# Kernel optimization log

Measured on AMD Instinct MI355X. Metric: run time of the kernel, lower is better.

Reference implementation:

```python
import jax, jax.numpy as jnp
import numpy as np

NUM_HEADS = 16


def setup_inputs() -> dict:
    key = jax.random.key(0)
    ks = jax.random.split(key, 8)
    B, S, E = 2, 2048, 1024
    std = 0.02
    return {
        "q": jax.random.normal(ks[0], (B, S, E), dtype=jnp.float32),
        "k": jax.random.normal(ks[1], (B, S, E), dtype=jnp.float32),
        "v": jax.random.normal(ks[2], (B, S, E), dtype=jnp.float32),
        "Wq": jax.random.normal(ks[3], (E, E), dtype=jnp.float32) * std,
        "Wk": jax.random.normal(ks[4], (E, E), dtype=jnp.float32) * std,
        "Wv": jax.random.normal(ks[5], (E, E), dtype=jnp.float32) * std,
        "Wo": jax.random.normal(ks[6], (E, E), dtype=jnp.float32) * std,
        "bo": jnp.zeros((E,), dtype=jnp.float32),
    }


def reference(q, k, v, Wq, Wk, Wv, Wo, bo):
    B, S, E = q.shape
    H = NUM_HEADS
    D = E // H
    # projections (nn.Linear: x @ W.T)
    Q = (q @ Wq.T).reshape(B, S, H, D).transpose(0, 2, 1, 3)  # [B,H,S,D]
    K = (k @ Wk.T).reshape(B, S, H, D).transpose(0, 2, 1, 3)
    V = (v @ Wv.T).reshape(B, S, H, D).transpose(0, 2, 1, 3)
    scores = jnp.einsum("bhsd,bhtd->bhst", Q, K)  # [B,H,S,S]
    # causal mask applied before scaling (as in source; -inf/sqrt(d) == -inf)
    causal = jnp.tril(jnp.ones((S, S), dtype=bool))
    scores = jnp.where(causal, scores, -jnp.inf)
    scores = scores / np.sqrt(D).astype(np.float32)
    attn = jax.nn.softmax(scores, axis=-1)
    out = jnp.einsum("bhst,bhtd->bhsd", attn, V)  # [B,H,S,D]
    out = out.transpose(0, 2, 1, 3).reshape(B, S, E)
    return out @ Wo.T + bo
```

## Files before the change

kernel.cpp:

```cpp
#include <hip/hip_runtime.h>

typedef unsigned short u16;
typedef __bf16 bf16x8 __attribute__((ext_vector_type(8)));
typedef float f32x4 __attribute__((ext_vector_type(4)));
typedef unsigned u32x4 __attribute__((ext_vector_type(4)));

#define B_ 2
#define S_ 2048
#define E_ 1024
#define H_ 16
#define D_ 64
#define M_ (B_ * S_)

__device__ inline u16 f2bf(float f) {
  union { float f; unsigned int u; } c; c.f = f;
  unsigned int u = c.u;
  return (u16)((u + 0x7FFFu + ((u >> 16) & 1u)) >> 16);
}

__device__ inline f32x4 mfma16(bf16x8 a, bf16x8 b, f32x4 c) {
  return __builtin_amdgcn_mfma_f32_16x16x32_bf16(a, b, c, 0, 0, 0);
}

__device__ inline void gload16(const void* g, void* lds) {
  __builtin_amdgcn_global_load_lds(
      (const __attribute__((address_space(1))) unsigned int*)g,
      (__attribute__((address_space(3))) unsigned int*)lds, 16, 0, 0);
}

struct CvtArgs {
  const float* src[7];
  u16* dst[7];
  int n[7];
};

__global__ __launch_bounds__(256) void cvt_kernel(CvtArgs a) {
  const int arr = blockIdx.y;
  const int n = a.n[arr];
  const float* __restrict__ s = a.src[arr];
  u16* __restrict__ d = a.dst[arr];
  const int stride = gridDim.x * blockDim.x;
  for (int i = blockIdx.x * blockDim.x + threadIdx.x; i * 4 < n; i += stride) {
    const float4 f = *(const float4*)(s + 4 * i);
    ushort4 o;
    o.x = f2bf(f.x); o.y = f2bf(f.y); o.z = f2bf(f.z); o.w = f2bf(f.w);
    *(ushort4*)(d + 4 * i) = o;
  }
}

__global__ __launch_bounds__(256, 4) void qkv_gemm(
    const u16* __restrict__ qb, const u16* __restrict__ kb,
    const u16* __restrict__ vbp, const u16* __restrict__ Wqb,
    const u16* __restrict__ Wkb, const u16* __restrict__ Wvb,
    u16* __restrict__ Qh, u16* __restrict__ Kh, u16* __restrict__ Vt) {
  constexpr int BM = 128, BN = 128, BK = 32;
  __shared__ alignas(16) u16 As[BM * BK];
  __shared__ alignas(16) u16 Bs[BN * BK];
  const int z = blockIdx.z;
  const u16* A  = (z == 0) ? qb  : (z == 1) ? kb  : vbp;
  const u16* Bt = (z == 0) ? Wqb : (z == 1) ? Wkb : Wvb;
  u16* outp     = (z == 0) ? Qh  : (z == 1) ? Kh  : Vt;

  const int tid = threadIdx.x;
  const int wave = tid >> 6, lane = tid & 63;
  const int m0 = blockIdx.y * BM, n0 = blockIdx.x * BN;
  const int wm = (wave >> 1) * 64, wn = (wave & 1) * 64;
  const int lrow = lane >> 2, lcol = (lane & 3) * 8;

  f32x4 acc[4][4] = {};

  for (int k0 = 0; k0 < E_; k0 += BK) {
#pragma unroll
    for (int i = 0; i < 2; ++i) {
      const int chunk = wave * 2 + i;
      const int row = chunk * 16 + lrow;
      gload16(A + (size_t)(m0 + row) * E_ + k0 + lcol, As + chunk * 16 * BK);
      gload16(Bt + (size_t)(n0 + row) * E_ + k0 + lcol, Bs + chunk * 16 * BK);
    }
    __syncthreads();
    bf16x8 af[4], bfr[4];
#pragma unroll
    for (int mi = 0; mi < 4; ++mi)
      af[mi] = *(const bf16x8*)&As[(wm + mi * 16 + (lane & 15)) * BK + 8 * (lane >> 4)];
#pragma unroll
    for (int ni = 0; ni < 4; ++ni)
      bfr[ni] = *(const bf16x8*)&Bs[(wn + ni * 16 + (lane & 15)) * BK + 8 * (lane >> 4)];
#pragma unroll
    for (int mi = 0; mi < 4; ++mi)
#pragma unroll
      for (int ni = 0; ni < 4; ++ni)
        acc[mi][ni] = mfma16(af[mi], bfr[ni], acc[mi][ni]);
    __syncthreads();
  }

#pragma unroll
  for (int mi = 0; mi < 4; ++mi)
#pragma unroll
    for (int ni = 0; ni < 4; ++ni)
#pragma unroll
      for (int r = 0; r < 4; ++r) {
        const int m = m0 + wm + mi * 16 + ((lane >> 4) << 2) + r;
        const int n = n0 + wn + ni * 16 + (lane & 15);
        const float v = acc[mi][ni][r];
        const int b = m >> 11, s = m & (S_ - 1), h = n >> 6, d = n & 63;
        if (z != 2) {
          outp[((((size_t)b * H_ + h) * S_ + s) << 6) + d] = f2bf(v);
        } else {
          outp[(((size_t)b * H_ + h) * D_ + d) * S_ + s] = f2bf(v);
        }
      }
}

__global__ __launch_bounds__(256, 4) void oproj_gemm(
    const u16* __restrict__ A, const u16* __restrict__ Bt,
    const float* __restrict__ bias, float* __restrict__ outp) {
  constexpr int BM = 64, BN = 128, BK = 32;
  constexpr int ACH = BM / 16, NCH = ACH + BN / 16;
  __shared__ alignas(16) u16 As[BM * BK];
  __shared__ alignas(16) u16 Bs[BN * BK];
  const int tid = threadIdx.x;
  const int wave = tid >> 6, lane = tid & 63;
  const int m0 = blockIdx.y * BM, n0 = blockIdx.x * BN;
  const int wm = (wave >> 1) * 32, wn = (wave & 1) * 64;
  const int lrow = lane >> 2, lcol = (lane & 3) * 8;

  f32x4 acc[2][4] = {};

  for (int k0 = 0; k0 < E_; k0 += BK) {
#pragma unroll
    for (int c = wave; c < NCH; c += 4) {
      if (c < ACH)
        gload16(A + (size_t)(m0 + c * 16 + lrow) * E_ + k0 + lcol, As + c * 16 * BK);
      else
        gload16(Bt + (size_t)(n0 + (c - ACH) * 16 + lrow) * E_ + k0 + lcol,
                Bs + (c - ACH) * 16 * BK);
    }
    __syncthreads();
    bf16x8 af[2], bfr[4];
#pragma unroll
    for (int mi = 0; mi < 2; ++mi)
      af[mi] = *(const bf16x8*)&As[(wm + mi * 16 + (lane & 15)) * BK + 8 * (lane >> 4)];
#pragma unroll
    for (int ni = 0; ni < 4; ++ni)
      bfr[ni] = *(const bf16x8*)&Bs[(wn + ni * 16 + (lane & 15)) * BK + 8 * (lane >> 4)];
#pragma unroll
    for (int mi = 0; mi < 2; ++mi)
#pragma unroll
      for (int ni = 0; ni < 4; ++ni)
        acc[mi][ni] = mfma16(af[mi], bfr[ni], acc[mi][ni]);
    __syncthreads();
  }

#pragma unroll
  for (int mi = 0; mi < 2; ++mi)
#pragma unroll
    for (int ni = 0; ni < 4; ++ni)
#pragma unroll
      for (int r = 0; r < 4; ++r) {
        const int m = m0 + wm + mi * 16 + ((lane >> 4) << 2) + r;
        const int n = n0 + wn + ni * 16 + (lane & 15);
        outp[(size_t)m * E_ + n] = acc[mi][ni][r] + bias[n];
      }
}


__device__ __forceinline__ void stage_kv(
    const u16* __restrict__ Kh_head, const u16* __restrict__ Vt_head,
    int kv0, u16* kb, u16* vb, int wq, int lane) {
#pragma unroll
  for (int i = 0; i < 2; ++i) {
    const int c = 2 * wq + i;
    gload16(Kh_head + (size_t)(kv0 + lane) * D_ + c * 8, kb + c * 512);
    gload16(Vt_head + (size_t)lane * S_ + kv0 + c * 8, vb + c * 512);
  }
}

__global__ __launch_bounds__(256, 2) void flash_attn(
    const u16* __restrict__ Qh, const u16* __restrict__ Kh,
    const u16* __restrict__ Vt, u16* __restrict__ O) {
  __shared__ alignas(16) u16 Kb[3][4096];
  __shared__ alignas(16) u16 Vb[3][4096];

  const int j = blockIdx.x;
  const int qt = 31 - (j >> 5);
  const int bh = j & 31;

  const int tid = threadIdx.x;
  const int wq = tid >> 6, lane = tid & 63;

  const int q0 = qt * 64;
  const int b = bh >> 4, h = bh & 15;
  constexpr float SC = 0.125f * 1.4426950408889634f;
  const int fr = lane & 15, fc = lane >> 4;

  const u16* Qbase = Qh + ((size_t)bh * S_ + q0 + wq * 16 + fr) * D_ + 8 * fc;
  const bf16x8 qf0 = *(const bf16x8*)Qbase;
  const bf16x8 qf1 = *(const bf16x8*)(Qbase + 32);
  const u16* Kh_head = Kh + (size_t)bh * S_ * D_;
  const u16* Vt_head = Vt + (size_t)bh * D_ * S_;

  float lacc = 0.f;
  f32x4 oacc[4] = {};
  const int nt = qt + 1;

  u16 *kA = Kb[0], *kB = Kb[1], *kC = Kb[2];
  u16 *vA = Vb[0], *vB = Vb[1], *vC = Vb[2];

  stage_kv(Kh_head, Vt_head, 0, kA, vA, wq, lane);
  stage_kv(Kh_head, Vt_head, 64, kB, vB, wq, lane);

  for (int t = 0; t < nt; ++t) {
    if (t + 1 < nt) {
      asm volatile("s_waitcnt vmcnt(4)" ::: "memory");
    } else {
      asm volatile("s_waitcnt vmcnt(0)" ::: "memory");
    }
    __builtin_amdgcn_s_barrier();
    __builtin_amdgcn_sched_barrier(0);

    if (t + 2 < nt)
      stage_kv(Kh_head, Vt_head, (t + 2) * 64, kC, vC, wq, lane);

    const u16* kb = kA;
    const u16* vb = vA;

    f32x4 sacc[4] = {};
    __builtin_amdgcn_s_setprio(1);
#pragma unroll
    for (int ni = 0; ni < 4; ++ni) {
      const bf16x8 k0 = *(const bf16x8*)&kb[fc * 512 + (16 * ni + fr) * 8];
      const bf16x8 k1 = *(const bf16x8*)&kb[(fc + 4) * 512 + (16 * ni + fr) * 8];
      sacc[ni] = mfma16(k0, qf0, sacc[ni]);
      sacc[ni] = mfma16(k1, qf1, sacc[ni]);
    }
    __builtin_amdgcn_s_setprio(0);

    const bool diag = (t == qt);
    const int qloc = wq * 16 + fr;
#pragma unroll
    for (int ni = 0; ni < 4; ++ni)
#pragma unroll
      for (int r = 0; r < 4; ++r) {
        const int kvloc = 16 * ni + 4 * fc + r;
        float pv;
        if (diag && kvloc > qloc) {
          pv = 0.f;
        } else {
          pv = __builtin_amdgcn_exp2f(sacc[ni][r] * SC);
        }
        sacc[ni][r] = pv;
        lacc += pv;
      }

    unsigned w[4][2];
#pragma unroll
    for (int ni = 0; ni < 4; ++ni) {
      asm("v_cvt_pk_bf16_f32 %0, %1, %2"
          : "=v"(w[ni][0]) : "v"(sacc[ni][0]), "v"(sacc[ni][1]));
      asm("v_cvt_pk_bf16_f32 %0, %1, %2"
          : "=v"(w[ni][1]) : "v"(sacc[ni][2]), "v"(sacc[ni][3]));
    }

    unsigned paw0[4], paw1[4];
#pragma unroll
    for (int pair = 0; pair < 2; ++pair) {
      unsigned xx[2], yy[2], tt[2];
#pragma unroll
      for (int hh = 0; hh < 2; ++hh) {
        unsigned a = w[2 * pair][hh], bb = w[2 * pair + 1][hh];
        asm volatile("v_permlane32_swap_b32 %0, %1" : "+v"(a), "+v"(bb));
        xx[hh] = a; yy[hh] = bb;
        const unsigned s = (fc & 1) ? a : bb;
        tt[hh] = (unsigned)__shfl_xor((int)s, 16);
      }
      unsigned* pw_ = pair ? paw1 : paw0;
      pw_[0] = (fc & 1) ? tt[0] : xx[0];
      pw_[1] = (fc & 1) ? tt[1] : xx[1];
      pw_[2] = (fc & 1) ? yy[0] : tt[0];
      pw_[3] = (fc & 1) ? yy[1] : tt[1];
    }
    bf16x8 pa0, pa1;
    {
      u32x4 t0 = {paw0[0], paw0[1], paw0[2], paw0[3]};
      u32x4 t1 = {paw1[0], paw1[1], paw1[2], paw1[3]};
      __builtin_memcpy(&pa0, &t0, 16);
      __builtin_memcpy(&pa1, &t1, 16);
    }

    __builtin_amdgcn_s_setprio(1);
#pragma unroll
    for (int nd = 0; nd < 4; ++nd) {
      const bf16x8 v0 = *(const bf16x8*)&vb[fc * 512 + (16 * nd + fr) * 8];
      const bf16x8 v1 = *(const bf16x8*)&vb[(fc + 4) * 512 + (16 * nd + fr) * 8];
      oacc[nd] = mfma16(pa0, v0, oacc[nd]);
      oacc[nd] = mfma16(pa1, v1, oacc[nd]);
    }
    __builtin_amdgcn_s_setprio(0);

    u16* tk = kA; kA = kB; kB = kC; kC = tk;
    u16* tv = vA; vA = vB; vB = vC; vC = tv;
  }

  float l = lacc;
  l += __shfl_xor(l, 16);
  l += __shfl_xor(l, 32);
  float linv[4];
#pragma unroll
  for (int r = 0; r < 4; ++r)
    linv[r] = __builtin_amdgcn_rcpf(__shfl(l, 4 * fc + r));

#pragma unroll
  for (int nd = 0; nd < 4; ++nd) {
#pragma unroll
    for (int r = 0; r < 4; ++r) {
      const int qr = q0 + wq * 16 + (fc << 2) + r;
      const int d = 16 * nd + fr;
      const float v = oacc[nd][r] * linv[r];
      O[((size_t)b * S_ + qr) * E_ + h * D_ + d] = f2bf(v);
    }
  }
}

extern "C" void kernel_launch(void* const* d_in, const int* in_sizes, int n_in,
                              void* d_out, int out_size, void* d_ws, size_t ws_size,
                              hipStream_t stream) {
  const float* q  = (const float*)d_in[0];
  const float* k  = (const float*)d_in[1];
  const float* v  = (const float*)d_in[2];
  const float* Wq = (const float*)d_in[3];
  const float* Wk = (const float*)d_in[4];
  const float* Wv = (const float*)d_in[5];
  const float* Wo = (const float*)d_in[6];
  const float* bo = (const float*)d_in[7];

  const size_t nBSE = (size_t)M_ * E_;
  const size_t nEE  = (size_t)E_ * E_;
  u16* qb  = (u16*)d_ws;
  u16* kb  = qb + nBSE;
  u16* vb  = kb + nBSE;
  u16* Wqb = vb + nBSE;
  u16* Wkb = Wqb + nEE;
  u16* Wvb = Wkb + nEE;
  u16* Wob = Wvb + nEE;
  u16* Qh  = Wob + nEE;
  u16* Kh  = Qh + nBSE;
  u16* Vt  = qb;
  u16* Oa  = vb;

  CvtArgs ca;
  ca.src[0] = q;  ca.dst[0] = qb;  ca.n[0] = (int)nBSE;
  ca.src[1] = k;  ca.dst[1] = kb;  ca.n[1] = (int)nBSE;
  ca.src[2] = v;  ca.dst[2] = vb;  ca.n[2] = (int)nBSE;
  ca.src[3] = Wq; ca.dst[3] = Wqb; ca.n[3] = (int)nEE;
  ca.src[4] = Wk; ca.dst[4] = Wkb; ca.n[4] = (int)nEE;
  ca.src[5] = Wv; ca.dst[5] = Wvb; ca.n[5] = (int)nEE;
  ca.src[6] = Wo; ca.dst[6] = Wob; ca.n[6] = (int)nEE;
  cvt_kernel<<<dim3(512, 7), 256, 0, stream>>>(ca);

  qkv_gemm<<<dim3(E_ / 128, M_ / 128, 3), 256, 0, stream>>>(
      qb, kb, vb, Wqb, Wkb, Wvb, Qh, Kh, Vt);
  flash_attn<<<dim3(1024), 256, 0, stream>>>(Qh, Kh, Vt, Oa);
  oproj_gemm<<<dim3(E_ / 128, M_ / 64), 256, 0, stream>>>(Oa, Wob, bo, (float*)d_out);
}
```

Baseline: 126.4 us.

## Triple-buffer QKV GEMM loads with swizzled LDS and XCD-aware block mapping

```diff
diff --git a/kernel.cpp b/kernel.cpp
--- a/kernel.cpp
+++ b/kernel.cpp
@@ -48,49 +48,82 @@
   }
 }
 
-__global__ __launch_bounds__(256, 4) void qkv_gemm(
+__global__ __launch_bounds__(256, 3) void qkv_gemm(
     const u16* __restrict__ qb, const u16* __restrict__ kb,
     const u16* __restrict__ vbp, const u16* __restrict__ Wqb,
     const u16* __restrict__ Wkb, const u16* __restrict__ Wvb,
     u16* __restrict__ Qh, u16* __restrict__ Kh, u16* __restrict__ Vt) {
   constexpr int BM = 128, BN = 128, BK = 32;
-  __shared__ alignas(16) u16 As[BM * BK];
-  __shared__ alignas(16) u16 Bs[BN * BK];
-  const int z = blockIdx.z;
+  __shared__ alignas(16) u16 As[3][BM * BK];
+  __shared__ alignas(16) u16 Bs[3][BN * BK];
+
+  const int wg = blockIdx.x;
+  const int xcd = wg & 7, idx = wg >> 3;
+  const int nb = idx & 7, mz = idx >> 3;
+  const int z = mz >> 2;
+  const int m0 = (xcd * 4 + (mz & 3)) * BM, n0 = nb * BN;
+
   const u16* A  = (z == 0) ? qb  : (z == 1) ? kb  : vbp;
   const u16* Bt = (z == 0) ? Wqb : (z == 1) ? Wkb : Wvb;
   u16* outp     = (z == 0) ? Qh  : (z == 1) ? Kh  : Vt;
 
   const int tid = threadIdx.x;
   const int wave = tid >> 6, lane = tid & 63;
-  const int m0 = blockIdx.y * BM, n0 = blockIdx.x * BN;
   const int wm = (wave >> 1) * 64, wn = (wave & 1) * 64;
-  const int lrow = lane >> 2, lcol = (lane & 3) * 8;
+  const int fr = lane & 15, fc = lane >> 4;
+  const int lrow = lane >> 2;
+  const int lcol_sw = (((lane & 3) ^ ((lrow >> 1) & 3)) * 8);
 
   f32x4 acc[4][4] = {};
 
-  for (int k0 = 0; k0 < E_; k0 += BK) {
+  u16 *aA = As[0], *aB = As[1], *aC = As[2];
+  u16 *bA = Bs[0], *bB = Bs[1], *bC = Bs[2];
+
+  auto stage = [&](int k0, u16* as, u16* bs) {
 #pragma unroll
     for (int i = 0; i < 2; ++i) {
       const int chunk = wave * 2 + i;
       const int row = chunk * 16 + lrow;
-      gload16(A + (size_t)(m0 + row) * E_ + k0 + lcol, As + chunk * 16 * BK);
-      gload16(Bt + (size_t)(n0 + row) * E_ + k0 + lcol, Bs + chunk * 16 * BK);
-    }
-    __syncthreads();
+      gload16(A + (size_t)(m0 + row) * E_ + k0 + lcol_sw, as + chunk * 16 * BK);
+      gload16(Bt + (size_t)(n0 + row) * E_ + k0 + lcol_sw, bs + chunk * 16 * BK);
+    }
+  };
+
+  constexpr int NK = E_ / BK;
+  stage(0, aA, bA);
+  stage(BK, aB, bB);
+
+  const int sl = (fc ^ ((fr >> 1) & 3)) * 8;
+
+  for (int t = 0; t < NK; ++t) {
+    if (t + 1 < NK) {
+      asm volatile("s_waitcnt vmcnt(4)" ::: "memory");
+    } else {
+      asm volatile("s_waitcnt vmcnt(0)" ::: "memory");
+    }
+    __builtin_amdgcn_s_barrier();
+    __builtin_amdgcn_sched_barrier(0);
+
+    if (t + 2 < NK) stage((t + 2) * BK, aC, bC);
+
     bf16x8 af[4], bfr[4];
 #pragma unroll
     for (int mi = 0; mi < 4; ++mi)
-      af[mi] = *(const bf16x8*)&As[(wm + mi * 16 + (lane & 15)) * BK + 8 * (lane >> 4)];
-#pragma unroll
-    for (int ni = 0; ni < 4; ++ni)
-      bfr[ni] = *(const bf16x8*)&Bs[(wn + ni * 16 + (lane & 15)) * BK + 8 * (lane >> 4)];
+      af[mi] = *(const bf16x8*)&aA[(wm + mi * 16 + fr) * BK + sl];
+#pragma unroll
+    for (int ni = 0; ni < 4; ++ni)
+      bfr[ni] = *(const bf16x8*)&bA[(wn + ni * 16 + fr) * BK + sl];
+    __builtin_amdgcn_s_setprio(1);
 #pragma unroll
     for (int mi = 0; mi < 4; ++mi)
 #pragma unroll
       for (int ni = 0; ni < 4; ++ni)
         acc[mi][ni] = mfma16(af[mi], bfr[ni], acc[mi][ni]);
-    __syncthreads();
+    __builtin_amdgcn_s_setprio(0);
+
+    u16* tp;
+    tp = aA; aA = aB; aB = aC; aC = tp;
+    tp = bA; bA = bB; bB = bC; bC = tp;
   }
 
 #pragma unroll
@@ -99,8 +132,8 @@
     for (int ni = 0; ni < 4; ++ni)
 #pragma unroll
       for (int r = 0; r < 4; ++r) {
-        const int m = m0 + wm + mi * 16 + ((lane >> 4) << 2) + r;
-        const int n = n0 + wn + ni * 16 + (lane & 15);
+        const int m = m0 + wm + mi * 16 + (fc << 2) + r;
+        const int n = n0 + wn + ni * 16 + fr;
         const float v = acc[mi][ni][r];
         const int b = m >> 11, s = m & (S_ - 1), h = n >> 6, d = n & 63;
         if (z != 2) {
@@ -162,7 +195,6 @@
         outp[(size_t)m * E_ + n] = acc[mi][ni][r] + bias[n];
       }
 }
-
 
 __device__ __forceinline__ void stage_kv(
     const u16* __restrict__ Kh_head, const u16* __restrict__ Vt_head,
@@ -357,7 +389,7 @@
   ca.src[6] = Wo; ca.dst[6] = Wob; ca.n[6] = (int)nEE;
   cvt_kernel<<<dim3(512, 7), 256, 0, stream>>>(ca);
 
-  qkv_gemm<<<dim3(E_ / 128, M_ / 128, 3), 256, 0, stream>>>(
+  qkv_gemm<<<dim3(768), 256, 0, stream>>>(
       qb, kb, vb, Wqb, Wkb, Wvb, Qh, Kh, Vt);
   flash_attn<<<dim3(1024), 256, 0, stream>>>(Qh, Kh, Vt, Oa);
   oproj_gemm<<<dim3(E_ / 128, M_ / 64), 256, 0, stream>>>(Oa, Wob, bo, (float*)d_out);
```

New measurement: 122.2 us. -3.3%, faster.
